# Performance work log

Hardware: AMD Instinct MI355X
Metric: run time of the kernel (lower is better)

## Reference

```python
import jax, jax.numpy as jnp
import numpy as np
from functools import partial

N, C, D, H, W = 2, 64, 8, 96, 96
G, K, PAD = 2, 3, 1
P = K ** 3
CG = C // G
AXIS_SCALE = jnp.array([0.5, 1.0, 1.0], dtype=jnp.float32)  # applied to (dx, dy, dz)
OFFSET_SCALE = 1.0  # converged warmup scale
EPS = 1e-5


def setup_inputs() -> dict:
    key = jax.random.key(0)
    ks = jax.random.split(key, 13)
    s = 0.05
    return {
        "x": jax.random.normal(ks[0], (N, C, D, H, W), jnp.float32),
        "w_pre": jax.random.normal(ks[1], (C, C), jnp.float32) * s,
        "w_in": jax.random.normal(ks[2], (C, C), jnp.float32) * s,
        "b_in": jnp.zeros((C,), jnp.float32),
        "w_dw": jax.random.normal(ks[3], (C, 1, K, K, K), jnp.float32) * s,
        "w_off": jax.random.normal(ks[4], (C, G * P * 3), jnp.float32) * s,
        "b_off": jnp.zeros((G * P * 3,), jnp.float32),
        "w_mask": jax.random.normal(ks[5], (C, G * P), jnp.float32) * s,
        "b_mask": jnp.zeros((G * P,), jnp.float32),
        "w_out": jax.random.normal(ks[6], (C, C), jnp.float32) * s,
        "b_out": jnp.zeros((C,), jnp.float32),
        "w_post": jax.random.normal(ks[7], (C, C), jnp.float32) * s,
        "gate": jnp.zeros((), jnp.float32),
    }


def _instance_norm(x):  # x: [N, C, D, H, W], normalize over spatial dims per (n, c)
    mean = jnp.mean(x, axis=(2, 3, 4), keepdims=True)
    var = jnp.var(x, axis=(2, 3, 4), keepdims=True)
    return (x - mean) * jax.lax.rsqrt(var + EPS)


def _dcn_core(x_proj, offset, mask):
    # x_proj: [N, D, H, W, C]; offset: [N, D, H, W, G, P, 3] (dx, dy, dz); mask: [N, D, H, W, G, P]
    Dp, Hp, Wp = D + 2 * PAD, H + 2 * PAD, W + 2 * PAD
    x_pad = jnp.pad(x_proj, ((0, 0), (PAD, PAD), (PAD, PAD), (PAD, PAD), (0, 0)))
    x_pad = x_pad.reshape(N, Dp, Hp, Wp, G, CG)

    n_idx = jnp.arange(N).reshape(N, 1, 1, 1, 1)
    g_idx = jnp.arange(G).reshape(1, 1, 1, 1, G)
    zg = jnp.arange(D, dtype=jnp.float32).reshape(1, D, 1, 1, 1)
    yg = jnp.arange(H, dtype=jnp.float32).reshape(1, 1, H, 1, 1)
    xg = jnp.arange(W, dtype=jnp.float32).reshape(1, 1, 1, W, 1)

    def trilinear(zs, ys, xs):  # each [N, D, H, W, G] float coords in padded frame
        z0 = jnp.floor(zs); y0 = jnp.floor(ys); x0 = jnp.floor(xs)
        fz = zs - z0; fy = ys - y0; fx = xs - x0
        z0i = z0.astype(jnp.int32); y0i = y0.astype(jnp.int32); x0i = x0.astype(jnp.int32)
        res = None
        for dz in (0, 1):
            wz = fz if dz else 1.0 - fz
            zi = z0i + dz
            for dy in (0, 1):
                wy = fy if dy else 1.0 - fy
                yi = y0i + dy
                for dx in (0, 1):
                    wx = fx if dx else 1.0 - fx
                    xi = x0i + dx
                    valid = ((zi >= 0) & (zi < Dp) & (yi >= 0) & (yi < Hp)
                             & (xi >= 0) & (xi < Wp)).astype(zs.dtype)
                    g = x_pad[n_idx, jnp.clip(zi, 0, Dp - 1), jnp.clip(yi, 0, Hp - 1),
                              jnp.clip(xi, 0, Wp - 1), g_idx]  # [N,D,H,W,G,CG]
                    term = g * (wz * wy * wx * valid)[..., None]
                    res = term if res is None else res + term
        return res

    # kernel grid points (z-major), base position in padded frame is out_idx + k_idx
    kk = jnp.arange(K, dtype=jnp.float32)
    kz, ky, kx = jnp.meshgrid(kk, kk, kk, indexing="ij")
    kpts = jnp.stack([kz.ravel(), ky.ravel(), kx.ravel()], axis=-1)  # [P, 3]

    off = offset * (AXIS_SCALE * OFFSET_SCALE)  # scale (dx, dy, dz)
    off_p = jnp.moveaxis(off, 5, 0)    # [P, N, D, H, W, G, 3]
    mask_p = jnp.moveaxis(mask, 5, 0)  # [P, N, D, H, W, G]

    def body(acc, inp):
        o, m, kp = inp
        zs = zg + kp[0] + o[..., 2]
        ys = yg + kp[1] + o[..., 1]
        xs = xg + kp[2] + o[..., 0]
        samp = trilinear(zs, ys, xs)  # [N,D,H,W,G,CG]
        return acc + m[..., None] * samp, None

    acc0 = jnp.zeros((N, D, H, W, G, CG), x_proj.dtype)
    acc, _ = jax.lax.scan(body, acc0, (off_p, mask_p, kpts))
    return acc.reshape(N, D, H, W, C)


def _forward(x, w_pre, w_in, b_in, w_dw, w_off, b_off, w_mask, b_mask, w_out, b_out, w_post, gate):
    pre = jnp.einsum("ncdhw,oc->nodhw", x, w_pre)  # 1x1x1 conv, no bias
    x_cl = jnp.transpose(pre, (0, 2, 3, 4, 1))     # [N,D,H,W,C]
    x_proj = x_cl @ w_in + b_in
    # depthwise 3x3x3 conv + InstanceNorm + GELU for the offset/mask branch
    dw = jax.lax.conv_general_dilated(
        pre, w_dw, window_strides=(1, 1, 1), padding=((PAD, PAD),) * 3,
        feature_group_count=C, dimension_numbers=("NCDHW", "OIDHW", "NCDHW"))
    dw = jax.nn.gelu(_instance_norm(dw))
    feat = jnp.transpose(dw, (0, 2, 3, 4, 1))      # [N,D,H,W,C]
    offset = (feat @ w_off + b_off).reshape(N, D, H, W, G, P, 3)
    mask = jax.nn.softmax((feat @ w_mask + b_mask).reshape(N, D, H, W, G, P), axis=-1)
    core = _dcn_core(x_proj, offset, mask)         # [N,D,H,W,C]
    out = core @ w_out + b_out
    y = jnp.transpose(out, (0, 4, 1, 2, 3))        # back to NCDHW
    y = jnp.einsum("ncdhw,oc->nodhw", y, w_post)   # post 1x1x1 conv
    return x + jax.nn.sigmoid(gate) * y


def reference(x, w_pre, w_in, b_in, w_dw, w_off, b_off, w_mask, b_mask, w_out, b_out, w_post, gate):
    return _forward(x, w_pre, w_in, b_in, w_dw, w_off, b_off, w_mask, b_mask, w_out, b_out, w_post, gate)
```

## Files before the change

### kernel.cpp

```cpp
#include <hip/hip_runtime.h>
#include <math.h>

#define N_ 2
#define C_ 64
#define D_ 8
#define H_ 96
#define W_ 96
#define S_ (D_*H_*W_)
#define HW_ (H_*W_)
#define ZP_ 12
#define YP_ 100
#define XP_ 100
#define NSTR_ (ZP_*YP_*XP_*64)
#define ZS_ (YP_*XP_*64)
#define YS_ (XP_*64)

typedef __attribute__((ext_vector_type(8))) short short8;
typedef __attribute__((ext_vector_type(4))) float f32x4;

__device__ __forceinline__ float gelu_fast(float x) {
    float a = 0.7978845608028654f * (x + 0.044715f*x*x*x);
    float E = __expf(2.f*a);
    return x - x * __builtin_amdgcn_rcpf(E + 1.f);
}

__device__ __forceinline__ unsigned short f2bf(float f) {
    unsigned u = __float_as_uint(f);
    unsigned r = (u + 0x7fffu + ((u >> 16) & 1u)) >> 16;
    return (unsigned short)r;
}

__device__ __forceinline__ unsigned pkhi(float a, float b) {
    return __builtin_amdgcn_perm(__float_as_uint(a), __float_as_uint(b), 0x07060302u);
}

__global__ __launch_bounds__(64) void k_prep(const float* __restrict__ w_out,
        const float* __restrict__ b_out, const float* __restrict__ w_post,
        const float* __restrict__ w_off, const float* __restrict__ b_off,
        const float* __restrict__ w_mask, const float* __restrict__ b_mask,
        float* __restrict__ W2, float* __restrict__ B2,
        unsigned short* __restrict__ wBg, float4* __restrict__ b4f) {
    int b = blockIdx.x;
    int t = threadIdx.x;
    float acc = 0.f;
    for (int c = 0; c < 64; ++c)
        acc = fmaf(w_out[b*64+c], w_post[t*64+c], acc);
    W2[b*64 + t] = acc;
    if (b == 0) {
        float a2 = 0.f;
        for (int c = 0; c < 64; ++c)
            a2 = fmaf(w_post[t*64+c], b_out[c], a2);
        B2[t] = a2;
    }
    {
        int c = b;
        for (int m = t; m < 224; m += 64) {
            float v = 0.f;
            if (m < 216) {
                int u = m >> 2, comp = m & 3;
                if (comp == 3) v = w_mask[c*54 + u];
                else {
                    v = w_off[c*162 + u*3 + comp];
                    if (comp == 0) v *= 0.5f;
                }
            }
            wBg[m*64 + c] = f2bf(v);
        }
    }
    if (b == 1 && t < 54)
        b4f[t] = make_float4(b_off[t*3]*0.5f, b_off[t*3+1], b_off[t*3+2], b_mask[t]);
}

__global__ __launch_bounds__(256) void k_pre_proj(const float* __restrict__ x,
        const float* __restrict__ w_pre, const float* __restrict__ w_in,
        const float* __restrict__ b_in, float* __restrict__ pre,
        unsigned short* __restrict__ xprojP) {
    __shared__ float lx[64][65];
    __shared__ float lwa[64][65];
    __shared__ float lwb[64][65];
    int b = blockIdx.x;
    int n = b / 1152;
    int s0 = (b % 1152) * 64;
    int tid = threadIdx.x;
    for (int idx = tid; idx < 1024; idx += 256) {
        int r = idx >> 4, q4 = (idx & 15) * 4;
        float4 vx = *(const float4*)&x[((size_t)(n*C_ + r))*S_ + s0 + q4];
        lx[r][q4] = vx.x; lx[r][q4+1] = vx.y; lx[r][q4+2] = vx.z; lx[r][q4+3] = vx.w;
        float4 va = *(const float4*)&w_pre[r*64 + q4];
        lwa[r][q4] = va.x; lwa[r][q4+1] = va.y; lwa[r][q4+2] = va.z; lwa[r][q4+3] = va.w;
        float4 vb = *(const float4*)&w_in[r*64 + q4];
        lwb[r][q4] = vb.x; lwb[r][q4+1] = vb.y; lwb[r][q4+2] = vb.z; lwb[r][q4+3] = vb.w;
    }
    __syncthreads();
    int o0 = (tid & 15) * 4;
    int v0 = (tid >> 4) * 4;
    float acc[4][4] = {};
    #pragma unroll 8
    for (int c = 0; c < 64; ++c) {
        float xv[4], wv[4];
        #pragma unroll
        for (int j = 0; j < 4; ++j) { xv[j] = lx[c][v0+j]; wv[j] = lwa[o0+j][c]; }
        #pragma unroll
        for (int vj = 0; vj < 4; ++vj)
            #pragma unroll
            for (int oj = 0; oj < 4; ++oj)
                acc[vj][oj] = fmaf(xv[vj], wv[oj], acc[vj][oj]);
    }
    #pragma unroll
    for (int vj = 0; vj < 4; ++vj) {
        float4 r = make_float4(acc[vj][0], acc[vj][1], acc[vj][2], acc[vj][3]);
        *(float4*)&pre[((size_t)(n*S_ + s0 + v0 + vj))*64 + o0] = r;
    }
    __syncthreads();
    #pragma unroll
    for (int vj = 0; vj < 4; ++vj)
        #pragma unroll
        for (int oj = 0; oj < 4; ++oj)
            lx[v0+vj][o0+oj] = acc[vj][oj];
    __syncthreads();
    float acc2[4][4];
    #pragma unroll
    for (int oj = 0; oj < 4; ++oj) {
        float bo = b_in[o0+oj];
        #pragma unroll
        for (int vj = 0; vj < 4; ++vj) acc2[vj][oj] = bo;
    }
    #pragma unroll 8
    for (int c = 0; c < 64; ++c) {
        float fv[4], wv[4];
        #pragma unroll
        for (int j = 0; j < 4; ++j) { fv[j] = lx[v0+j][c]; wv[j] = lwb[c][o0+j]; }
        #pragma unroll
        for (int vj = 0; vj < 4; ++vj)
            #pragma unroll
            for (int oj = 0; oj < 4; ++oj)
                acc2[vj][oj] = fmaf(fv[vj], wv[oj], acc2[vj][oj]);
    }
    #pragma unroll
    for (int vj = 0; vj < 4; ++vj) {
        int vox = s0 + v0 + vj;
        int z = vox / HW_;
        int rem = vox - z*HW_;
        int y = rem / W_;
        int xq = rem - y*W_;
        size_t pw = (size_t)n*NSTR_ + (size_t)(z+2)*ZS_ + (y+2)*YS_ + (xq+2)*64 + o0;
        ushort4 pk;
        pk.x = f2bf(acc2[vj][0]); pk.y = f2bf(acc2[vj][1]);
        pk.z = f2bf(acc2[vj][2]); pk.w = f2bf(acc2[vj][3]);
        *(ushort4*)&xprojP[pw] = pk;
    }
}

__global__ __launch_bounds__(256) void k_dw_stats(const float* __restrict__ pre,
        const float* __restrict__ w_dw, float* __restrict__ dw,
        float* __restrict__ psum, float* __restrict__ pss) {
    __shared__ float4 lwd[27][16];
    __shared__ float4 lsum[16][16];
    __shared__ float4 lssum[16][16];
    int b = blockIdx.x;
    int y = b % H_;
    int z = (b / H_) % D_;
    int n = b / (D_*H_);
    int tid = threadIdx.x;
    if (tid < 27*16) {
        int k = tid >> 4, c4 = tid & 15;
        lwd[k][c4] = make_float4(w_dw[(c4*4+0)*27 + k], w_dw[(c4*4+1)*27 + k],
                                 w_dw[(c4*4+2)*27 + k], w_dw[(c4*4+3)*27 + k]);
    }
    __syncthreads();
    int c4 = tid & 15, xg = tid >> 4;
    const float* preN = pre + (size_t)n*S_*64;
    float4 s4 = make_float4(0,0,0,0), ss4 = make_float4(0,0,0,0);
    for (int xx = 0; xx < 6; ++xx) {
        int xi = xg + xx*16;
        float4 acc = make_float4(0,0,0,0);
        #pragma unroll
        for (int dz = 0; dz < 3; ++dz) {
            int zz = z + dz - 1;
            if (zz < 0 || zz >= D_) continue;
            #pragma unroll
            for (int dy = 0; dy < 3; ++dy) {
                int yy = y + dy - 1;
                if (yy < 0 || yy >= H_) continue;
                int rowb = (zz*HW_ + yy*W_)*64 + c4*4;
                #pragma unroll
                for (int dx = 0; dx < 3; ++dx) {
                    int xn = xi + dx - 1;
                    if ((unsigned)xn < (unsigned)W_) {
                        float4 v = *(const float4*)&preN[rowb + (xn<<6)];
                        float4 w = lwd[dz*9+dy*3+dx][c4];
                        acc.x = fmaf(v.x, w.x, acc.x);
                        acc.y = fmaf(v.y, w.y, acc.y);
                        acc.z = fmaf(v.z, w.z, acc.z);
                        acc.w = fmaf(v.w, w.w, acc.w);
                    }
                }
            }
        }
        *(float4*)&dw[((size_t)n*S_ + z*HW_ + y*W_ + xi)*64 + c4*4] = acc;
        s4.x += acc.x; s4.y += acc.y; s4.z += acc.z; s4.w += acc.w;
        ss4.x = fmaf(acc.x, acc.x, ss4.x); ss4.y = fmaf(acc.y, acc.y, ss4.y);
        ss4.z = fmaf(acc.z, acc.z, ss4.z); ss4.w = fmaf(acc.w, acc.w, ss4.w);
    }
    lsum[xg][c4] = s4; lssum[xg][c4] = ss4;
    __syncthreads();
    if (tid < 64) {
        float s = 0.f, ss = 0.f;
        #pragma unroll
        for (int k = 0; k < 16; ++k) {
            s  += ((const float*)&lsum [k][tid>>2])[tid&3];
            ss += ((const float*)&lssum[k][tid>>2])[tid&3];
        }
        psum[tid*1536 + b] = s;
        pss [tid*1536 + b] = ss;
    }
}

__global__ void k_stats2(const float* __restrict__ psum, const float* __restrict__ pss,
                         float* __restrict__ stats) {
    int u = blockIdx.x;
    int n = u >> 6, c = u & 63;
    int l = threadIdx.x;
    float s = 0.f, ss = 0.f;
    #pragma unroll
    for (int k = 0; k < 12; ++k) {
        int row = n*768 + k*64 + l;
        s  += psum[c*1536 + row];
        ss += pss [c*1536 + row];
    }
    #pragma unroll
    for (int o2 = 32; o2 >= 1; o2 >>= 1) {
        s  += __shfl_xor(s, o2);
        ss += __shfl_xor(ss, o2);
    }
    if (l == 0) {
        float inv = 1.f / (float)S_;
        float mean = s * inv;
        float var = ss * inv - mean*mean;
        stats[n*128 + c] = mean;
        stats[n*128 + 64 + c] = rsqrtf(var + 1e-5f);
    }
}

__global__ __launch_bounds__(256) void k_dcn(const unsigned short* __restrict__ xprojP,
        const float* __restrict__ dw, const float* __restrict__ stats,
        const unsigned short* __restrict__ wBg, const float4* __restrict__ b4f,
        unsigned short* __restrict__ coreB) {
    __shared__ union {
        unsigned short featB[32][64];
        int cwl[64][27];
    } uS;
    __shared__ float4 offs4[64][29];
    int tid = threadIdx.x;
    int orig = blockIdx.x;
    int bid = (orig & 7) * 576 + (orig >> 3);
    int x8 = bid % 12;
    int t1 = bid / 12;
    int y4 = t1 % 24;
    int t2 = t1 / 24;
    int z  = t2 & 7;
    int n  = t2 >> 3;
    int yb = y4*4, xb = x8*8;
    size_t voxBase = (size_t)n*S_ + (size_t)z*HW_ + yb*W_ + xb;

    {
        int c4 = (tid & 15) * 4;
        int vp = tid >> 4;
        #pragma unroll
        for (int j = 0; j < 2; ++j) {
            int vloc = vp*2 + j;
            size_t vox = voxBase + (vloc>>3)*W_ + (vloc & 7);
            float4 v = *(const float4*)&dw[vox*64 + c4];
            float vals[4] = {v.x, v.y, v.z, v.w};
            ushort4 pk;
            unsigned short* pp = (unsigned short*)&pk;
            #pragma unroll
            for (int jj = 0; jj < 4; ++jj) {
                int c = c4 + jj;
                float t = (vals[jj] - stats[n*128+c]) * stats[n*128+64+c];
                pp[jj] = f2bf(gelu_fast(t));
            }
            int off = ((((c4 >> 3) ^ (vloc & 7)) << 3) | (c4 & 7));
            *(ushort4*)&uS.featB[vloc][off] = pk;
        }
    }
    __syncthreads();

    {
        int w = tid >> 6;
        int l = tid & 63;
        int lr = l & 15;
        int lq = l >> 4;
        for (int i = 0; i < 7; ++i) {
            int t7 = w*7 + i;
            int mt = t7 >> 1, nt = t7 & 1;
            int vox = nt*16 + lr;
            f32x4 acc = {0.f, 0.f, 0.f, 0.f};
            #pragma unroll
            for (int h = 0; h < 2; ++h) {
                int k0 = h*32 + lq*8;
                short8 af = *(const short8*)&wBg[(mt*16 + lr)*64 + k0];
                int blk = (((k0 >> 3) ^ (vox & 7)) << 3);
                short8 bf = *(const short8*)&uS.featB[vox][blk];
                acc = __builtin_amdgcn_mfma_f32_16x16x32_bf16(af, bf, acc, 0, 0, 0);
            }
            int u = mt*4 + lq;
            if (u < 54) {
                float4 bb = b4f[u];
                int g = (u >= 27) ? 1 : 0;
                int p = u - g*27;
                offs4[vox*2 + g][p] = make_float4(acc[0] + bb.x, acc[1] + bb.y,
                                                  acc[2] + bb.z, acc[3] + bb.w);
            }
        }
    }
    __syncthreads();

    if (tid < 64) {
        float mx = -1e30f;
        #pragma unroll
        for (int p = 0; p < 27; ++p) mx = fmaxf(mx, offs4[tid][p].w);
        float e[27]; float ssum = 0.f;
        #pragma unroll
        for (int p = 0; p < 27; ++p) { e[p] = __expf(offs4[tid][p].w - mx); ssum += e[p]; }
        float inv = __builtin_amdgcn_rcpf(ssum);
        #pragma unroll
        for (int p = 0; p < 27; ++p) offs4[tid][p].w = e[p]*inv;
    }
    __syncthreads();

    {
        int zm1 = z - 1;
        #pragma unroll
        for (int k = 0; k < 7; ++k) {
            int idx = tid + k*256;
            if (idx < 1728) {
                int pair = idx / 27;
                int p = idx - pair*27;
                float4 tp = offs4[pair][p];
                int vloc = pair >> 1, g = pair & 1;
                int yy = vloc >> 3, xx = vloc & 7;
                float zf = (float)(zm1 + p/9) + tp.z;
                float yf = (float)(yb + yy - 1 + (p/3)%3) + tp.y;
                float xf = (float)(xb + xx - 1 + p%3) + tp.x;
                zf = fminf(fmaxf(zf, -1.5f), (float)D_ + 0.5f);
                yf = fminf(fmaxf(yf, -1.5f), (float)H_ + 0.5f);
                xf = fminf(fmaxf(xf, -1.5f), (float)W_ + 0.5f);
                float z0f = floorf(zf), y0f = floorf(yf), x0f = floorf(xf);
                float fz = zf - z0f, fy = yf - y0f, fx = xf - x0f;
                int zi = (int)z0f, yi = (int)y0f, xi = (int)x0f;
                float wz1 = fz * tp.w, wz0 = tp.w - wz1;
                float wy1 = fy, wy0 = 1.f - fy;
                float wx1 = fx, wx0 = 1.f - fx;
                float w00 = wz0*wy0, w01 = wz0*wy1, w10 = wz1*wy0, w11 = wz1*wy1;
                unsigned u0 = pkhi(w00*wx1, w00*wx0);
                unsigned u1 = pkhi(w01*wx1, w01*wx0);
                unsigned u2 = pkhi(w10*wx1, w10*wx0);
                unsigned u3 = pkhi(w11*wx1, w11*wx0);
                int cw = zi*ZS_ + yi*YS_ + (xi<<6) + (2*ZS_ + 2*YS_ + 128) + g*32;
                *(uint4*)&offs4[pair][p] = make_uint4(u0,u1,u2,u3);
                uS.cwl[pair][p] = cw;
            }
        }
    }
    __syncthreads();

    int pair = tid >> 2;
    int vloc = pair >> 1, g = pair & 1;
    int yy = vloc >> 3, xx = vloc & 7;
    int ch4 = (tid & 3) * 8;
    const unsigned short* __restrict__ base = xprojP + (size_t)n*NSTR_ + ch4;
    float a0=0.f,a1=0.f,a2=0.f,a3=0.f,a4=0.f,a5=0.f,a6=0.f,a7=0.f;
    #pragma unroll
    for (int p = 0; p < 27; ++p) {
        uint4 dsc = *(const uint4*)&offs4[pair][p];
        int cw = uS.cwl[pair][p];
        const unsigned short* p00 = base + cw;
        const unsigned short* p01 = p00 + YS_;
        const unsigned short* p10 = p00 + ZS_;
        const unsigned short* p11 = p10 + YS_;
        uint4 q000 = *(const uint4*)p00;
        uint4 q001 = *(const uint4*)(p00 + 64);
        uint4 q010 = *(const uint4*)p01;
        uint4 q011 = *(const uint4*)(p01 + 64);
        uint4 q100 = *(const uint4*)p10;
        uint4 q101 = *(const uint4*)(p10 + 64);
        uint4 q110 = *(const uint4*)p11;
        uint4 q111 = *(const uint4*)(p11 + 64);
        float c000 = __uint_as_float(dsc.x << 16), c001 = __uint_as_float(dsc.x);
        float c010 = __uint_as_float(dsc.y << 16), c011 = __uint_as_float(dsc.y);
        float c100 = __uint_as_float(dsc.z << 16), c101 = __uint_as_float(dsc.z);
        float c110 = __uint_as_float(dsc.w << 16), c111 = __uint_as_float(dsc.w);
        #define ACC8(Q, WGT) { \
            float wq = (WGT); \
            a0 = fmaf(wq, __uint_as_float((Q).x << 16), a0); \
            a1 = fmaf(wq, __uint_as_float((Q).x), a1); \
            a2 = fmaf(wq, __uint_as_float((Q).y << 16), a2); \
            a3 = fmaf(wq, __uint_as_float((Q).y), a3); \
            a4 = fmaf(wq, __uint_as_float((Q).z << 16), a4); \
            a5 = fmaf(wq, __uint_as_float((Q).z), a5); \
            a6 = fmaf(wq, __uint_as_float((Q).w << 16), a6); \
            a7 = fmaf(wq, __uint_as_float((Q).w), a7); \
        }
        ACC8(q000, c000); ACC8(q001, c001); ACC8(q010, c010); ACC8(q011, c011);
        ACC8(q100, c100); ACC8(q101, c101); ACC8(q110, c110); ACC8(q111, c111);
        #undef ACC8
    }
    size_t voxOut = voxBase + yy*W_ + xx;
    unsigned r01 = pkhi(a1, a0);
    unsigned r23 = pkhi(a3, a2);
    unsigned r45 = pkhi(a5, a4);
    unsigned r67 = pkhi(a7, a6);
    *(uint4*)&coreB[voxOut*64 + g*32 + ch4] = make_uint4(r01, r23, r45, r67);
}

__global__ __launch_bounds__(256) void k_final(const unsigned short* __restrict__ coreB,
        const float* __restrict__ W2, const float* __restrict__ B2,
        const float* __restrict__ x, const float* __restrict__ gate,
        float* __restrict__ out) {
    __shared__ float lc[64][65];
    __shared__ float lw[64][65];
    int b = blockIdx.x;
    int n = b / 1152;
    int s0 = (b % 1152) * 64;
    int tid = threadIdx.x;
    for (int idx = tid; idx < 512; idx += 256) {
        int r = idx >> 3, q8 = (idx & 7) * 8;
        uint4 q = *(const uint4*)&coreB[((size_t)(n*S_ + s0 + r))*64 + q8];
        lc[r][q8+0] = __uint_as_float(q.x << 16);
        lc[r][q8+1] = __uint_as_float(q.x & 0xffff0000u);
        lc[r][q8+2] = __uint_as_float(q.y << 16);
        lc[r][q8+3] = __uint_as_float(q.y & 0xffff0000u);
        lc[r][q8+4] = __uint_as_float(q.z << 16);
        lc[r][q8+5] = __uint_as_float(q.z & 0xffff0000u);
        lc[r][q8+6] = __uint_as_float(q.w << 16);
        lc[r][q8+7] = __uint_as_float(q.w & 0xffff0000u);
    }
    for (int idx = tid; idx < 1024; idx += 256) {
        int r = idx >> 4, q4 = (idx & 15) * 4;
        float4 vw = *(const float4*)&W2[r*64 + q4];
        lw[r][q4] = vw.x; lw[r][q4+1] = vw.y; lw[r][q4+2] = vw.z; lw[r][q4+3] = vw.w;
    }
    __syncthreads();
    float sg = 1.f / (1.f + expf(-gate[0]));
    int o0 = (tid & 15) * 4;
    int v0 = (tid >> 4) * 4;
    float acc[4][4];
    #pragma unroll
    for (int oj = 0; oj < 4; ++oj) {
        float bo = B2[o0+oj];
        #pragma unroll
        for (int vj = 0; vj < 4; ++vj) acc[vj][oj] = bo;
    }
    #pragma unroll 8
    for (int c = 0; c < 64; ++c) {
        float fv[4], wv[4];
        #pragma unroll
        for (int j = 0; j < 4; ++j) { fv[j] = lc[v0+j][c]; wv[j] = lw[c][o0+j]; }
        #pragma unroll
        for (int vj = 0; vj < 4; ++vj)
            #pragma unroll
            for (int oj = 0; oj < 4; ++oj)
                acc[vj][oj] = fmaf(fv[vj], wv[oj], acc[vj][oj]);
    }
    #pragma unroll
    for (int oj = 0; oj < 4; ++oj) {
        size_t gi = ((size_t)(n*64 + o0 + oj))*S_ + s0 + v0;
        float4 xv = *(const float4*)&x[gi];
        float4 r;
        r.x = fmaf(sg, acc[0][oj], xv.x);
        r.y = fmaf(sg, acc[1][oj], xv.y);
        r.z = fmaf(sg, acc[2][oj], xv.z);
        r.w = fmaf(sg, acc[3][oj], xv.w);
        *(float4*)&out[gi] = r;
    }
}

extern "C" void kernel_launch(void* const* d_in, const int* in_sizes, int n_in,
                              void* d_out, int out_size, void* d_ws, size_t ws_size,
                              hipStream_t stream) {
    const float* x      = (const float*)d_in[0];
    const float* w_pre  = (const float*)d_in[1];
    const float* w_in   = (const float*)d_in[2];
    const float* b_in   = (const float*)d_in[3];
    const float* w_dw   = (const float*)d_in[4];
    const float* w_off  = (const float*)d_in[5];
    const float* b_off  = (const float*)d_in[6];
    const float* w_mask = (const float*)d_in[7];
    const float* b_mask = (const float*)d_in[8];
    const float* w_out  = (const float*)d_in[9];
    const float* b_out  = (const float*)d_in[10];
    const float* w_post = (const float*)d_in[11];
    const float* gate   = (const float*)d_in[12];
    float* out = (float*)d_out;

    float* ws      = (float*)d_ws;
    unsigned short* xprojP = (unsigned short*)ws;
    float* pre     = ws + (size_t)7680000;
    unsigned short* coreB = (unsigned short*)(pre + (size_t)9437184);
    float* psum    = (float*)(coreB + (size_t)9437184);
    float* pss     = psum + 98304;
    float* stats   = pss + 98304;
    float* W2      = stats + 256;
    float* B2      = W2 + 4096;
    unsigned short* wBg = (unsigned short*)(B2 + 128);
    float4* b4f    = (float4*)(B2 + 128 + 7168);
    float* dwb     = out;

    hipMemsetAsync(xprojP, 0, (size_t)15360000*sizeof(unsigned short), stream);
    hipLaunchKernelGGL(k_prep,     dim3(64),   dim3(64),  0, stream,
                       w_out, b_out, w_post, w_off, b_off, w_mask, b_mask,
                       W2, B2, wBg, b4f);
    hipLaunchKernelGGL(k_pre_proj, dim3(2304), dim3(256), 0, stream,
                       x, w_pre, w_in, b_in, pre, xprojP);
    hipLaunchKernelGGL(k_dw_stats, dim3(1536), dim3(256), 0, stream,
                       pre, w_dw, dwb, psum, pss);
    hipLaunchKernelGGL(k_stats2,   dim3(128),  dim3(64),  0, stream, psum, pss, stats);
    hipLaunchKernelGGL(k_dcn,      dim3(4608), dim3(256), 0, stream,
                       xprojP, dwb, stats, wBg, b4f, coreB);
    hipLaunchKernelGGL(k_final,    dim3(2304), dim3(256), 0, stream,
                       coreB, W2, B2, x, gate, out);
}
```

Measured before the change: 324.5 us.

## Fuse output projection into DCN kernel with MFMA and fp16 dot2 sampling

```diff
diff --git a/kernel.cpp b/kernel.cpp
--- a/kernel.cpp
+++ b/kernel.cpp
@@ -17,6 +17,20 @@
 
 typedef __attribute__((ext_vector_type(8))) short short8;
 typedef __attribute__((ext_vector_type(4))) float f32x4;
+typedef __attribute__((ext_vector_type(2))) __fp16 h2;
+
+union U32H2 { unsigned u; h2 h; unsigned short s[2]; };
+__device__ __forceinline__ h2 uAsH2(unsigned u){ U32H2 t; t.u = u; return t.h; }
+__device__ __forceinline__ unsigned h2AsU(h2 h){ U32H2 t; t.h = h; return t.u; }
+
+__device__ __forceinline__ float dot2f(unsigned u, h2 w, float acc) {
+#if __has_builtin(__builtin_amdgcn_fdot2)
+    return __builtin_amdgcn_fdot2(uAsH2(u), w, acc, false);
+#else
+    h2 v = uAsH2(u);
+    return fmaf((float)v.y, (float)w.y, fmaf((float)v.x, (float)w.x, acc));
+#endif
+}
 
 __device__ __forceinline__ float gelu_fast(float x) {
     float a = 0.7978845608028654f * (x + 0.044715f*x*x*x);
@@ -30,22 +44,22 @@
     return (unsigned short)r;
 }
 
-__device__ __forceinline__ unsigned pkhi(float a, float b) {
-    return __builtin_amdgcn_perm(__float_as_uint(a), __float_as_uint(b), 0x07060302u);
+__device__ __forceinline__ unsigned short f2h(float f) {
+    U32H2 t; t.h[0] = (__fp16)f; t.h[1] = (__fp16)0.f; return t.s[0];
 }
 
 __global__ __launch_bounds__(64) void k_prep(const float* __restrict__ w_out,
         const float* __restrict__ b_out, const float* __restrict__ w_post,
         const float* __restrict__ w_off, const float* __restrict__ b_off,
         const float* __restrict__ w_mask, const float* __restrict__ b_mask,
-        float* __restrict__ W2, float* __restrict__ B2,
+        float* __restrict__ B2, unsigned short* __restrict__ W2T,
         unsigned short* __restrict__ wBg, float4* __restrict__ b4f) {
     int b = blockIdx.x;
     int t = threadIdx.x;
     float acc = 0.f;
     for (int c = 0; c < 64; ++c)
         acc = fmaf(w_out[b*64+c], w_post[t*64+c], acc);
-    W2[b*64 + t] = acc;
+    W2T[t*64 + b] = f2h(acc);
     if (b == 0) {
         float a2 = 0.f;
         for (int c = 0; c < 64; ++c)
@@ -144,10 +158,9 @@
         int y = rem / W_;
         int xq = rem - y*W_;
         size_t pw = (size_t)n*NSTR_ + (size_t)(z+2)*ZS_ + (y+2)*YS_ + (xq+2)*64 + o0;
-        ushort4 pk;
-        pk.x = f2bf(acc2[vj][0]); pk.y = f2bf(acc2[vj][1]);
-        pk.z = f2bf(acc2[vj][2]); pk.w = f2bf(acc2[vj][3]);
-        *(ushort4*)&xprojP[pw] = pk;
+        unsigned lo = h2AsU(__builtin_amdgcn_cvt_pkrtz(acc2[vj][0], acc2[vj][1]));
+        unsigned hi = h2AsU(__builtin_amdgcn_cvt_pkrtz(acc2[vj][2], acc2[vj][3]));
+        *(uint2*)&xprojP[pw] = make_uint2(lo, hi);
     }
 }
 
@@ -245,12 +258,15 @@
 __global__ __launch_bounds__(256) void k_dcn(const unsigned short* __restrict__ xprojP,
         const float* __restrict__ dw, const float* __restrict__ stats,
         const unsigned short* __restrict__ wBg, const float4* __restrict__ b4f,
-        unsigned short* __restrict__ coreB) {
+        const unsigned short* __restrict__ W2T, const float* __restrict__ B2,
+        const float* __restrict__ xin, const float* __restrict__ gate,
+        float* __restrict__ out) {
+    __shared__ uint4 descW[27][64];
     __shared__ union {
         unsigned short featB[32][64];
-        int cwl[64][27];
+        int cwl[27][64];
+        unsigned short coreT[32][64];
     } uS;
-    __shared__ float4 offs4[64][29];
     int tid = threadIdx.x;
     int orig = blockIdx.x;
     int bid = (orig & 7) * 576 + (orig >> 3);
@@ -262,6 +278,7 @@
     int n  = t2 >> 3;
     int yb = y4*4, xb = x8*8;
     size_t voxBase = (size_t)n*S_ + (size_t)z*HW_ + yb*W_ + xb;
+    float4* offsF = (float4*)descW;
 
     {
         int c4 = (tid & 15) * 4;
@@ -309,23 +326,31 @@
                 float4 bb = b4f[u];
                 int g = (u >= 27) ? 1 : 0;
                 int p = u - g*27;
-                offs4[vox*2 + g][p] = make_float4(acc[0] + bb.x, acc[1] + bb.y,
-                                                  acc[2] + bb.z, acc[3] + bb.w);
+                offsF[p*64 + vox*2 + g] = make_float4(acc[0] + bb.x, acc[1] + bb.y,
+                                                      acc[2] + bb.z, acc[3] + bb.w);
             }
         }
     }
     __syncthreads();
 
     if (tid < 64) {
+        int pair = tid;
         float mx = -1e30f;
         #pragma unroll
-        for (int p = 0; p < 27; ++p) mx = fmaxf(mx, offs4[tid][p].w);
+        for (int p = 0; p < 27; ++p) mx = fmaxf(mx, offsF[p*64 + pair].w);
         float e[27]; float ssum = 0.f;
         #pragma unroll
-        for (int p = 0; p < 27; ++p) { e[p] = __expf(offs4[tid][p].w - mx); ssum += e[p]; }
+        for (int p = 0; p < 27; ++p) {
+            e[p] = __expf(offsF[p*64 + pair].w - mx);
+            ssum += e[p];
+        }
         float inv = __builtin_amdgcn_rcpf(ssum);
         #pragma unroll
-        for (int p = 0; p < 27; ++p) offs4[tid][p].w = e[p]*inv;
+        for (int p = 0; p < 27; ++p) {
+            float4 t = offsF[p*64 + pair];
+            t.w = e[p]*inv;
+            offsF[p*64 + pair] = t;
+        }
     }
     __syncthreads();
 
@@ -335,9 +360,9 @@
         for (int k = 0; k < 7; ++k) {
             int idx = tid + k*256;
             if (idx < 1728) {
-                int pair = idx / 27;
-                int p = idx - pair*27;
-                float4 tp = offs4[pair][p];
+                int pair = idx & 63;
+                int p = idx >> 6;
+                float4 tp = offsF[p*64 + pair];
                 int vloc = pair >> 1, g = pair & 1;
                 int yy = vloc >> 3, xx = vloc & 7;
                 float zf = (float)(zm1 + p/9) + tp.z;
@@ -353,13 +378,13 @@
                 float wy1 = fy, wy0 = 1.f - fy;
                 float wx1 = fx, wx0 = 1.f - fx;
                 float w00 = wz0*wy0, w01 = wz0*wy1, w10 = wz1*wy0, w11 = wz1*wy1;
-                unsigned u0 = pkhi(w00*wx1, w00*wx0);
-                unsigned u1 = pkhi(w01*wx1, w01*wx0);
-                unsigned u2 = pkhi(w10*wx1, w10*wx0);
-                unsigned u3 = pkhi(w11*wx1, w11*wx0);
+                unsigned u0 = h2AsU(__builtin_amdgcn_cvt_pkrtz(w00*wx0, w00*wx1));
+                unsigned u1 = h2AsU(__builtin_amdgcn_cvt_pkrtz(w01*wx0, w01*wx1));
+                unsigned u2 = h2AsU(__builtin_amdgcn_cvt_pkrtz(w10*wx0, w10*wx1));
+                unsigned u3 = h2AsU(__builtin_amdgcn_cvt_pkrtz(w11*wx0, w11*wx1));
                 int cw = zi*ZS_ + yi*YS_ + (xi<<6) + (2*ZS_ + 2*YS_ + 128) + g*32;
-                *(uint4*)&offs4[pair][p] = make_uint4(u0,u1,u2,u3);
-                uS.cwl[pair][p] = cw;
+                descW[p][pair] = make_uint4(u0, u1, u2, u3);
+                uS.cwl[p][pair] = cw;
             }
         }
     }
@@ -367,112 +392,82 @@
 
     int pair = tid >> 2;
     int vloc = pair >> 1, g = pair & 1;
-    int yy = vloc >> 3, xx = vloc & 7;
     int ch4 = (tid & 3) * 8;
     const unsigned short* __restrict__ base = xprojP + (size_t)n*NSTR_ + ch4;
     float a0=0.f,a1=0.f,a2=0.f,a3=0.f,a4=0.f,a5=0.f,a6=0.f,a7=0.f;
     #pragma unroll
     for (int p = 0; p < 27; ++p) {
-        uint4 dsc = *(const uint4*)&offs4[pair][p];
-        int cw = uS.cwl[pair][p];
+        uint4 wp = descW[p][pair];
+        int cw = uS.cwl[p][pair];
         const unsigned short* p00 = base + cw;
         const unsigned short* p01 = p00 + YS_;
         const unsigned short* p10 = p00 + ZS_;
         const unsigned short* p11 = p10 + YS_;
-        uint4 q000 = *(const uint4*)p00;
-        uint4 q001 = *(const uint4*)(p00 + 64);
-        uint4 q010 = *(const uint4*)p01;
-        uint4 q011 = *(const uint4*)(p01 + 64);
-        uint4 q100 = *(const uint4*)p10;
-        uint4 q101 = *(const uint4*)(p10 + 64);
-        uint4 q110 = *(const uint4*)p11;
-        uint4 q111 = *(const uint4*)(p11 + 64);
-        float c000 = __uint_as_float(dsc.x << 16), c001 = __uint_as_float(dsc.x);
-        float c010 = __uint_as_float(dsc.y << 16), c011 = __uint_as_float(dsc.y);
-        float c100 = __uint_as_float(dsc.z << 16), c101 = __uint_as_float(dsc.z);
-        float c110 = __uint_as_float(dsc.w << 16), c111 = __uint_as_float(dsc.w);
-        #define ACC8(Q, WGT) { \
-            float wq = (WGT); \
-            a0 = fmaf(wq, __uint_as_float((Q).x << 16), a0); \
-            a1 = fmaf(wq, __uint_as_float((Q).x), a1); \
-            a2 = fmaf(wq, __uint_as_float((Q).y << 16), a2); \
-            a3 = fmaf(wq, __uint_as_float((Q).y), a3); \
-            a4 = fmaf(wq, __uint_as_float((Q).z << 16), a4); \
-            a5 = fmaf(wq, __uint_as_float((Q).z), a5); \
-            a6 = fmaf(wq, __uint_as_float((Q).w << 16), a6); \
-            a7 = fmaf(wq, __uint_as_float((Q).w), a7); \
-        }
-        ACC8(q000, c000); ACC8(q001, c001); ACC8(q010, c010); ACC8(q011, c011);
-        ACC8(q100, c100); ACC8(q101, c101); ACC8(q110, c110); ACC8(q111, c111);
-        #undef ACC8
-    }
-    size_t voxOut = voxBase + yy*W_ + xx;
-    unsigned r01 = pkhi(a1, a0);
-    unsigned r23 = pkhi(a3, a2);
-    unsigned r45 = pkhi(a5, a4);
-    unsigned r67 = pkhi(a7, a6);
-    *(uint4*)&coreB[voxOut*64 + g*32 + ch4] = make_uint4(r01, r23, r45, r67);
-}
-
-__global__ __launch_bounds__(256) void k_final(const unsigned short* __restrict__ coreB,
-        const float* __restrict__ W2, const float* __restrict__ B2,
-        const float* __restrict__ x, const float* __restrict__ gate,
-        float* __restrict__ out) {
-    __shared__ float lc[64][65];
-    __shared__ float lw[64][65];
-    int b = blockIdx.x;
-    int n = b / 1152;
-    int s0 = (b % 1152) * 64;
-    int tid = threadIdx.x;
-    for (int idx = tid; idx < 512; idx += 256) {
-        int r = idx >> 3, q8 = (idx & 7) * 8;
-        uint4 q = *(const uint4*)&coreB[((size_t)(n*S_ + s0 + r))*64 + q8];
-        lc[r][q8+0] = __uint_as_float(q.x << 16);
-        lc[r][q8+1] = __uint_as_float(q.x & 0xffff0000u);
-        lc[r][q8+2] = __uint_as_float(q.y << 16);
-        lc[r][q8+3] = __uint_as_float(q.y & 0xffff0000u);
-        lc[r][q8+4] = __uint_as_float(q.z << 16);
-        lc[r][q8+5] = __uint_as_float(q.z & 0xffff0000u);
-        lc[r][q8+6] = __uint_as_float(q.w << 16);
-        lc[r][q8+7] = __uint_as_float(q.w & 0xffff0000u);
-    }
-    for (int idx = tid; idx < 1024; idx += 256) {
-        int r = idx >> 4, q4 = (idx & 15) * 4;
-        float4 vw = *(const float4*)&W2[r*64 + q4];
-        lw[r][q4] = vw.x; lw[r][q4+1] = vw.y; lw[r][q4+2] = vw.z; lw[r][q4+3] = vw.w;
-    }
-    __syncthreads();
-    float sg = 1.f / (1.f + expf(-gate[0]));
-    int o0 = (tid & 15) * 4;
-    int v0 = (tid >> 4) * 4;
-    float acc[4][4];
-    #pragma unroll
-    for (int oj = 0; oj < 4; ++oj) {
-        float bo = B2[o0+oj];
-        #pragma unroll
-        for (int vj = 0; vj < 4; ++vj) acc[vj][oj] = bo;
-    }
-    #pragma unroll 8
-    for (int c = 0; c < 64; ++c) {
-        float fv[4], wv[4];
-        #pragma unroll
-        for (int j = 0; j < 4; ++j) { fv[j] = lc[v0+j][c]; wv[j] = lw[c][o0+j]; }
-        #pragma unroll
-        for (int vj = 0; vj < 4; ++vj)
+        uint4 qa0 = *(const uint4*)p00;
+        uint4 qa1 = *(const uint4*)(p00 + 64);
+        uint4 qb0 = *(const uint4*)p01;
+        uint4 qb1 = *(const uint4*)(p01 + 64);
+        uint4 qc0 = *(const uint4*)p10;
+        uint4 qc1 = *(const uint4*)(p10 + 64);
+        uint4 qd0 = *(const uint4*)p11;
+        uint4 qd1 = *(const uint4*)(p11 + 64);
+        h2 w0 = uAsH2(wp.x), w1 = uAsH2(wp.y), w2 = uAsH2(wp.z), w3 = uAsH2(wp.w);
+        #define CP(QA, QB, WH) { \
+            a0 = dot2f(__builtin_amdgcn_perm(QA.x, QB.x, 0x01000504u), WH, a0); \
+            a1 = dot2f(__builtin_amdgcn_perm(QA.x, QB.x, 0x03020706u), WH, a1); \
+            a2 = dot2f(__builtin_amdgcn_perm(QA.y, QB.y, 0x01000504u), WH, a2); \
+            a3 = dot2f(__builtin_amdgcn_perm(QA.y, QB.y, 0x03020706u), WH, a3); \
+            a4 = dot2f(__builtin_amdgcn_perm(QA.z, QB.z, 0x01000504u), WH, a4); \
+            a5 = dot2f(__builtin_amdgcn_perm(QA.z, QB.z, 0x03020706u), WH, a5); \
+            a6 = dot2f(__builtin_amdgcn_perm(QA.w, QB.w, 0x01000504u), WH, a6); \
+            a7 = dot2f(__builtin_amdgcn_perm(QA.w, QB.w, 0x03020706u), WH, a7); \
+        }
+        CP(qa0, qa1, w0); CP(qb0, qb1, w1); CP(qc0, qc1, w2); CP(qd0, qd1, w3);
+        #undef CP
+    }
+    __syncthreads();
+
+    {
+        unsigned c01 = h2AsU(__builtin_amdgcn_cvt_pkrtz(a0, a1));
+        unsigned c23 = h2AsU(__builtin_amdgcn_cvt_pkrtz(a2, a3));
+        unsigned c45 = h2AsU(__builtin_amdgcn_cvt_pkrtz(a4, a5));
+        unsigned c67 = h2AsU(__builtin_amdgcn_cvt_pkrtz(a6, a7));
+        int col = g*32 + ch4;
+        int blk = (((col >> 3) ^ (vloc & 7)) << 3);
+        *(uint4*)&uS.coreT[vloc][blk] = make_uint4(c01, c23, c45, c67);
+    }
+    __syncthreads();
+
+    {
+        int w = tid >> 6, l = tid & 63, lr = l & 15, lq = l >> 4;
+        float sg = 1.f / (1.f + __expf(-gate[0]));
+        #pragma unroll
+        for (int t = 0; t < 2; ++t) {
+            int tile = w*2 + t;
+            int mt = tile >> 2, nt = tile & 3;
+            int o = nt*16 + lr;
+            f32x4 acc = {0.f, 0.f, 0.f, 0.f};
             #pragma unroll
-            for (int oj = 0; oj < 4; ++oj)
-                acc[vj][oj] = fmaf(fv[vj], wv[oj], acc[vj][oj]);
-    }
-    #pragma unroll
-    for (int oj = 0; oj < 4; ++oj) {
-        size_t gi = ((size_t)(n*64 + o0 + oj))*S_ + s0 + v0;
-        float4 xv = *(const float4*)&x[gi];
-        float4 r;
-        r.x = fmaf(sg, acc[0][oj], xv.x);
-        r.y = fmaf(sg, acc[1][oj], xv.y);
-        r.z = fmaf(sg, acc[2][oj], xv.z);
-        r.w = fmaf(sg, acc[3][oj], xv.w);
-        *(float4*)&out[gi] = r;
+            for (int h = 0; h < 2; ++h) {
+                int k0 = h*32 + lq*8;
+                int arow = mt*16 + lr;
+                int blk = (((k0 >> 3) ^ (arow & 7)) << 3);
+                short8 af = *(const short8*)&uS.coreT[arow][blk];
+                short8 bf = *(const short8*)&W2T[o*64 + k0];
+                acc = __builtin_amdgcn_mfma_f32_16x16x32_f16(af, bf, acc, 0, 0, 0);
+            }
+            float b2 = B2[o];
+            int vox0 = mt*16 + lq*4;
+            int yy = vox0 >> 3, xx0 = vox0 & 7;
+            size_t gi = ((size_t)(n*64 + o))*S_ + (size_t)z*HW_ + (size_t)(yb+yy)*W_ + (xb+xx0);
+            float4 xv = *(const float4*)&xin[gi];
+            float4 r;
+            r.x = fmaf(sg, acc[0] + b2, xv.x);
+            r.y = fmaf(sg, acc[1] + b2, xv.y);
+            r.z = fmaf(sg, acc[2] + b2, xv.z);
+            r.w = fmaf(sg, acc[3] + b2, xv.w);
+            *(float4*)&out[gi] = r;
+        }
     }
 }
 
@@ -497,27 +492,24 @@
     float* ws      = (float*)d_ws;
     unsigned short* xprojP = (unsigned short*)ws;
     float* pre     = ws + (size_t)7680000;
-    unsigned short* coreB = (unsigned short*)(pre + (size_t)9437184);
-    float* psum    = (float*)(coreB + (size_t)9437184);
+    float* dwb     = pre + (size_t)9437184;
+    float* psum    = dwb + (size_t)9437184;
     float* pss     = psum + 98304;
     float* stats   = pss + 98304;
-    float* W2      = stats + 256;
-    float* B2      = W2 + 4096;
-    unsigned short* wBg = (unsigned short*)(B2 + 128);
-    float4* b4f    = (float4*)(B2 + 128 + 7168);
-    float* dwb     = out;
-
-    hipMemsetAsync(xprojP, 0, (size_t)15360000*sizeof(unsigned short), stream);
+    float* B2      = stats + 256;
+    unsigned short* W2T = (unsigned short*)(B2 + 128);
+    unsigned short* wBg = W2T + 4096;
+    float4* b4f    = (float4*)(wBg + 14336 + 64);
+
+    (void)hipMemsetAsync(xprojP, 0, (size_t)15360000*sizeof(unsigned short), stream);
     hipLaunchKernelGGL(k_prep,     dim3(64),   dim3(64),  0, stream,
                        w_out, b_out, w_post, w_off, b_off, w_mask, b_mask,
-                       W2, B2, wBg, b4f);
+                       B2, W2T, wBg, b4f);
     hipLaunchKernelGGL(k_pre_proj, dim3(2304), dim3(256), 0, stream,
                        x, w_pre, w_in, b_in, pre, xprojP);
     hipLaunchKernelGGL(k_dw_stats, dim3(1536), dim3(256), 0, stream,
                        pre, w_dw, dwb, psum, pss);
     hipLaunchKernelGGL(k_stats2,   dim3(128),  dim3(64),  0, stream, psum, pss, stats);
     hipLaunchKernelGGL(k_dcn,      dim3(4608), dim3(256), 0, stream,
-                       xprojP, dwb, stats, wBg, b4f, coreB);
-    hipLaunchKernelGGL(k_final,    dim3(2304), dim3(256), 0, stream,
-                       coreB, W2, B2, x, gate, out);
-}
+                       xprojP, dwb, stats, wBg, b4f, W2T, B2, x, gate, out);
+}
```

After: 314.6 us. 1.03x faster.
